# Kernel optimization log

Hardware: AMD Instinct MI355X
Metric: run time of the kernel (lower is better)

The kernel has to match this reference:

```python
import jax, jax.numpy as jnp
import numpy as np

D_MODEL = 1024
NUM_HEADS = 16
DEPTH = D_MODEL // NUM_HEADS
B, S = 2, 2048
NEG = -1e9


def setup_inputs() -> dict:
    key = jax.random.key(0)
    ks = jax.random.split(key, 12)
    sc = 1.0 / np.sqrt(D_MODEL)
    inp = {
        "query": jax.random.normal(ks[0], (B, S, D_MODEL), jnp.float32),
        "key_in": jax.random.normal(ks[1], (B, S, D_MODEL), jnp.float32),
        "value": jax.random.normal(ks[2], (B, S, D_MODEL), jnp.float32),
        # causal mask: 1.0 where attention is disallowed (upper triangle)
        "mask": (1.0 - jnp.tril(jnp.ones((S, S), jnp.float32)))[None, None, :, :],
        "wq": jax.random.normal(ks[3], (D_MODEL, D_MODEL), jnp.float32) * sc,
        "bq": jnp.zeros((D_MODEL,), jnp.float32),
        "wk": jax.random.normal(ks[4], (D_MODEL, D_MODEL), jnp.float32) * sc,
        "bk": jnp.zeros((D_MODEL,), jnp.float32),
        "wv": jax.random.normal(ks[5], (D_MODEL, D_MODEL), jnp.float32) * sc,
        "bv": jnp.zeros((D_MODEL,), jnp.float32),
        "wo": jax.random.normal(ks[6], (D_MODEL, D_MODEL), jnp.float32) * sc,
        "bo": jnp.zeros((D_MODEL,), jnp.float32),
    }
    return inp


def _split_heads(x):
    # [B,S,D] -> [B,H,S,depth]
    b, s, _ = x.shape
    return x.reshape(b, s, NUM_HEADS, DEPTH).transpose(0, 2, 1, 3)


def reference(query, key_in, value, mask, wq, bq, wk, bk, wv, bv, wo, bo):
    q = _split_heads(query @ wq + bq)
    k = _split_heads(key_in @ wk + bk)
    v = _split_heads(value @ wv + bv)
    scale = 1.0 / jnp.sqrt(jnp.asarray(DEPTH, jnp.float32))
    logits = jnp.einsum("bhqd,bhkd->bhqk", q, k) * scale + mask * NEG
    attn = jax.nn.softmax(logits, axis=-1)
    out = jnp.einsum("bhqk,bhkd->bhqd", attn, v)  # [B,H,S,depth]
    out = out.transpose(0, 2, 1, 3).reshape(query.shape[0], -1, D_MODEL)
    return out @ wo + bo
```

## Files before the change

### kernel.cpp

```cpp
#include <hip/hip_runtime.h>
#include <hip/hip_bf16.h>
#include <cstdint>
#include <cstddef>

#define D_MODEL 1024
#define NHEADS  16
#define DEPTH   64
#define BATCH   2
#define SEQ     2048
#define M_TOT   (BATCH*SEQ)
#define QK_SCALE 0.18033688011112042f

typedef __attribute__((ext_vector_type(8)))  __bf16 bf16x8;
typedef __attribute__((ext_vector_type(4)))  float  f32x4;
typedef __attribute__((ext_vector_type(16))) float  f32x16;

__device__ inline unsigned short f2bf(float f){
  unsigned u = __float_as_uint(f);
  u += 0x7FFFu + ((u>>16)&1u);
  return (unsigned short)(u>>16);
}
__device__ inline unsigned cvtpk(float lo, float hi){
  unsigned r;
  asm("v_cvt_pk_bf16_f32 %0, %1, %2" : "=v"(r) : "v"(lo), "v"(hi));
  return r;
}
__device__ inline float fexp2(float x){
  float r;
  asm("v_exp_f32 %0, %1" : "=v"(r) : "v"(x));
  return r;
}
__device__ inline int bswap23(int x){
  return (x & ~12) | ((x & 4) << 1) | ((x & 8) >> 1);
}

#define AS1(p) ((__attribute__((address_space(1))) void*)(p))
#define AS3(p) ((__attribute__((address_space(3))) void*)(p))

__device__ inline void bar_vm4(){
  asm volatile("s_waitcnt vmcnt(4)" ::: "memory");
  __builtin_amdgcn_s_barrier();
  __builtin_amdgcn_sched_barrier(0);
}
__device__ inline void bar_lg(){
  asm volatile("s_waitcnt lgkmcnt(0)" ::: "memory");
  __builtin_amdgcn_s_barrier();
  __builtin_amdgcn_sched_barrier(0);
}

__global__ void tcvt4(const float* __restrict__ w0, const float* __restrict__ w1,
                      const float* __restrict__ w2, const float* __restrict__ w3,
                      unsigned short* o0, unsigned short* o1,
                      unsigned short* o2, unsigned short* o3){
  const float* W = blockIdx.z==0 ? w0 : blockIdx.z==1 ? w1 : blockIdx.z==2 ? w2 : w3;
  unsigned short* Wt = blockIdx.z==0 ? o0 : blockIdx.z==1 ? o1 : blockIdx.z==2 ? o2 : o3;
  const bool perm = (blockIdx.z == 3);
  __shared__ float t[32][33];
  int bx = blockIdx.x*32, by = blockIdx.y*32;
  for (int j = threadIdx.y; j < 32; j += 8)
    t[j][threadIdx.x] = W[(size_t)(by+j)*D_MODEL + bx + threadIdx.x];
  __syncthreads();
  for (int j = threadIdx.y; j < 32; j += 8){
    int col = by + threadIdx.x;
    if (perm) col = bswap23(col);
    Wt[(size_t)(bx+j)*D_MODEL + col] = f2bf(t[threadIdx.x][j]);
  }
}

#define BM 128
#define BN 128
#define BK 32
#define GK 1024

__global__ __launch_bounds__(256,2) void gemm_qkv(
    const float* __restrict__ Xfq, const float* __restrict__ Xfk,
    const float* __restrict__ Xfv,
    const unsigned short* __restrict__ Wq, const unsigned short* __restrict__ Wk,
    const unsigned short* __restrict__ Wv,
    const float* __restrict__ bq, const float* __restrict__ bk, const float* __restrict__ bv,
    unsigned short* Qh, unsigned short* Kh, unsigned short* Vth)
{
  __shared__ __align__(16) short As[BM*BK];
  __shared__ __align__(16) short Bs[2][BN*BK];
  const int z = blockIdx.z;
  const float* Af          = z==0 ? Xfq : z==1 ? Xfk : Xfv;
  const unsigned short* Bt = z==0 ? Wq  : z==1 ? Wk  : Wv;
  const float* bias        = z==0 ? bq  : z==1 ? bk  : bv;

  const int tid = threadIdx.x, lane = tid & 63, wave = tid >> 6;
  const int m0 = blockIdx.x*BM, n0 = blockIdx.y*BN;
  const int wm = wave >> 1, wn = wave & 1;

  f32x4 acc[4][4];
  #pragma unroll
  for (int i=0;i<4;i++)
    #pragma unroll
    for (int j=0;j<4;j++)
      acc[i][j] = (f32x4){0.f,0.f,0.f,0.f};

  const char* Afb   = (const char*)Af + (size_t)m0*GK*4;
  const char* Bbase = (const char*)Bt + (size_t)n0*GK*2;
  const int arow = tid >> 2;
  const int acb  = (tid & 3) * 32;

  float4 alo0[2], ahi0[2], alo1[2], ahi1[2];

#define LOADA(LO, HI, k0) \
  _Pragma("unroll") \
  for (int c=0;c<2;c++){ \
    const char* p_ = Afb + (size_t)(c*64 + arow)*(GK*4) + (size_t)(k0)*4 + acb; \
    LO[c] = *(const float4*)p_; HI[c] = *(const float4*)(p_ + 16); }

#define ISSUEB(t) \
  _Pragma("unroll") \
  for (int c=0;c<2;c++) \
    __builtin_amdgcn_global_load_lds( \
      AS1(Bbase + (size_t)(c*64 + arow)*(GK*2) + (t)*64 + (tid&3)*16), \
      AS3((char*)&Bs[(t)&1][0] + c*4096 + tid*16), 16, 0, 0);

#define CVT_WR(LO, HI) { \
    uint4 pk_[2]; \
    _Pragma("unroll") \
    for (int c=0;c<2;c++){ \
      pk_[c].x = cvtpk(LO[c].x, LO[c].y); pk_[c].y = cvtpk(LO[c].z, LO[c].w); \
      pk_[c].z = cvtpk(HI[c].x, HI[c].y); pk_[c].w = cvtpk(HI[c].z, HI[c].w); } \
    bar_vm4(); \
    _Pragma("unroll") \
    for (int c=0;c<2;c++) *(uint4*)((char*)As + c*4096 + tid*16) = pk_[c]; \
    bar_lg(); }

#define CVT_WR_SYNC(LO, HI) { \
    uint4 pk_[2]; \
    _Pragma("unroll") \
    for (int c=0;c<2;c++){ \
      pk_[c].x = cvtpk(LO[c].x, LO[c].y); pk_[c].y = cvtpk(LO[c].z, LO[c].w); \
      pk_[c].z = cvtpk(HI[c].x, HI[c].y); pk_[c].w = cvtpk(HI[c].z, HI[c].w); } \
    __syncthreads(); \
    _Pragma("unroll") \
    for (int c=0;c<2;c++) *(uint4*)((char*)As + c*4096 + tid*16) = pk_[c]; \
    __syncthreads(); }

#define MFMA_PHASE(BUF) { \
    bf16x8 af_[4], bfv_[4]; \
    _Pragma("unroll") \
    for (int i=0;i<4;i++) \
      af_[i] = *(const bf16x8*)((const char*)As + (wm*64+i*16+(lane&15))*64 + (lane>>4)*16); \
    _Pragma("unroll") \
    for (int j=0;j<4;j++) \
      bfv_[j] = *(const bf16x8*)((const char*)&Bs[BUF][0] + (wn*64+j*16+(lane&15))*64 + (lane>>4)*16); \
    _Pragma("unroll") \
    for (int i=0;i<4;i++) \
      _Pragma("unroll") \
      for (int j=0;j<4;j++) \
        acc[i][j] = __builtin_amdgcn_mfma_f32_16x16x32_bf16(af_[i], bfv_[j], acc[i][j], 0,0,0); }

  ISSUEB(0)
  __builtin_amdgcn_sched_barrier(0);
  LOADA(alo0, ahi0, 0)
  LOADA(alo1, ahi1, 32)

  #pragma unroll 1
  for (int k0 = 0; k0 < 960; k0 += 64){
    const int t = k0 >> 5;
    CVT_WR(alo0, ahi0)
    ISSUEB(t+1)
    __builtin_amdgcn_sched_barrier(0);
    LOADA(alo0, ahi0, k0+64)
    MFMA_PHASE(t&1)
    CVT_WR(alo1, ahi1)
    ISSUEB(t+2)
    __builtin_amdgcn_sched_barrier(0);
    LOADA(alo1, ahi1, k0+96)
    MFMA_PHASE((t+1)&1)
  }
  CVT_WR_SYNC(alo0, ahi0)
  ISSUEB(31)
  MFMA_PHASE(0)
  CVT_WR_SYNC(alo1, ahi1)
  MFMA_PHASE(1)

  #pragma unroll
  for (int i=0;i<4;i++)
    #pragma unroll
    for (int j=0;j<4;j++)
      #pragma unroll
      for (int r=0;r<4;r++){
        int gr = m0 + wm*64 + i*16 + (lane>>4)*4 + r;
        int gc = n0 + wn*64 + j*16 + (lane&15);
        float v = acc[i][j][r] + bias[gc];
        int b = gr>>11, s = gr&2047, h = gc>>6, d = gc&63;
        if (z == 0){
          v *= QK_SCALE;
          Qh[(((size_t)(b*NHEADS+h))*SEQ + s)*DEPTH + d] = f2bf(v);
        } else if (z == 1){
          Kh[(((size_t)(b*NHEADS+h))*SEQ + s)*DEPTH + d] = f2bf(v);
        } else {
          int sp = bswap23(s);
          Vth[(((size_t)(b*NHEADS+h))*DEPTH + d)*SEQ + sp] = f2bf(v);
        }
      }
#undef LOADA
#undef ISSUEB
#undef CVT_WR
#undef CVT_WR_SYNC
#undef MFMA_PHASE
}

#define BM2 64
__global__ __launch_bounds__(256,2) void gemm_out(
    const unsigned short* __restrict__ A,
    const unsigned short* __restrict__ Bt,
    const float* __restrict__ bias,
    float* __restrict__ Cout)
{
  __shared__ __align__(16) short As[2][BM2*BK];
  __shared__ __align__(16) short Bs[2][BN*BK];
  const int tid = threadIdx.x, lane = tid & 63, wave = tid >> 6;
  const int m0 = blockIdx.x*BM2, n0 = blockIdx.y*BN;
  const int wm = wave >> 1, wn = wave & 1;

  f32x4 acc[2][4];
  #pragma unroll
  for (int i=0;i<2;i++)
    #pragma unroll
    for (int j=0;j<4;j++)
      acc[i][j] = (f32x4){0.f,0.f,0.f,0.f};

  const char* Abase = (const char*)A + (size_t)m0*GK*2;
  const char* Bbase = (const char*)Bt + (size_t)n0*GK*2;

  auto STAGE = [&](int t){
    __builtin_amdgcn_global_load_lds(
      AS1(Abase + (size_t)(tid>>2)*(GK*2) + t*64 + (tid&3)*16),
      AS3((char*)&As[t&1][0] + tid*16), 16, 0, 0);
    #pragma unroll
    for (int c=0;c<2;c++)
      __builtin_amdgcn_global_load_lds(
        AS1(Bbase + (size_t)(c*64 + (tid>>2))*(GK*2) + t*64 + (tid&3)*16),
        AS3((char*)&Bs[t&1][0] + c*4096 + tid*16), 16, 0, 0);
  };

  STAGE(0);
  #pragma unroll 1
  for (int t = 0; t < 32; ++t){
    __syncthreads();
    if (t+1 < 32) STAGE(t+1);
    bf16x8 af[2], bfv[4];
    #pragma unroll
    for (int i=0;i<2;i++)
      af[i] = *(const bf16x8*)((const char*)&As[t&1][0] + (wm*32 + i*16 + (lane&15))*64 + (lane>>4)*16);
    #pragma unroll
    for (int j=0;j<4;j++)
      bfv[j] = *(const bf16x8*)((const char*)&Bs[t&1][0] + (wn*64 + j*16 + (lane&15))*64 + (lane>>4)*16);
    #pragma unroll
    for (int i=0;i<2;i++)
      #pragma unroll
      for (int j=0;j<4;j++)
        acc[i][j] = __builtin_amdgcn_mfma_f32_16x16x32_bf16(af[i], bfv[j], acc[i][j], 0,0,0);
  }

  #pragma unroll
  for (int i=0;i<2;i++)
    #pragma unroll
    for (int j=0;j<4;j++)
      #pragma unroll
      for (int r=0;r<4;r++){
        int gr = m0 + wm*32 + i*16 + (lane>>4)*4 + r;
        int gc = n0 + wn*64 + j*16 + (lane&15);
        Cout[(size_t)gr*D_MODEL + gc] = acc[i][j][r] + bias[gc];
      }
}

__global__ __launch_bounds__(512,4) void attn_fwd(
  const unsigned short* __restrict__ Qh,
  const unsigned short* __restrict__ Kh,
  const unsigned short* __restrict__ Vt,
  unsigned short* __restrict__ AO)
{
  __shared__ __align__(16) short Ks[2][4096];
  __shared__ __align__(16) short Vs[2][4096];
  __shared__ float cbS[2][128];

  const int tid = threadIdx.x, lane = tid & 63, w = tid >> 6;
  const int h = lane >> 5, ql = lane & 31;
  const int qh = w & 1, kh = (w >> 1) & 1, tl = w >> 2;
  const int pj = blockIdx.x, bh = blockIdx.y;
  const size_t hb = (size_t)bh * SEQ * DEPTH;
  const char* Kb = (const char*)(Kh + hb);
  const char* Vb = (const char*)(Vt + hb);
  const unsigned short* Qb = Qh + hb;
  const int bb = bh >> 4, hd = bh & 15;
  const int swz = (ql & 7) << 4;

  auto STAGE = [&](int buf, int t){
    const int kv0 = t*64;
    #pragma unroll
    for (int i=0;i<2;i++){
      int c = (w&3)*2 + i;
      int x = c*1024 + lane*16;
      int row = x >> 7;
      int cb = (x & 127) ^ ((row&7)<<4);
      if (w < 4)
        __builtin_amdgcn_global_load_lds(
          AS1(Kb + (size_t)(kv0+row)*128 + cb),
          AS3((char*)&Ks[buf][0] + c*1024), 16, 0, 0);
      else
        __builtin_amdgcn_global_load_lds(
          AS1(Vb + ((size_t)row*SEQ + kv0)*2 + cb),
          AS3((char*)&Vs[buf][0] + c*1024), 16, 0, 0);
    }
  };

  const int jtw = tl ? pj : (31 - pj);
  const int Q0 = jtw*64 + qh*32;
  const int qmax = Q0 + 31;
  const int Tblock = 32 - pj;

  bf16x8 qreg[4];
  {
    const unsigned short* qp = Qb + (size_t)(Q0 + ql)*DEPTH + h*8;
    #pragma unroll
    for (int c=0;c<4;c++) qreg[c] = *(const bf16x8*)(qp + c*16);
  }

  f32x16 oacc[2];
  #pragma unroll
  for (int dh=0;dh<2;dh++)
    #pragma unroll
    for (int r=0;r<16;r++) oacc[dh][r] = 0.f;
  float s = 0.f;

  STAGE(0, 0);
  __syncthreads();
  int cur = 0;

  #pragma unroll 1
  for (int t = 0; t < Tblock; ++t){
    if (t+1 < Tblock) STAGE(cur^1, t+1);
    const int kvb = t*64 + kh*32;

    if (kvb <= qmax){
      f32x16 sa;
      #pragma unroll
      for (int r=0;r<16;r++) sa[r] = -16.0f;
      #pragma unroll
      for (int c=0;c<4;c++){
        bf16x8 kf = *(const bf16x8*)((const char*)&Ks[cur][0]
                      + (kh*32 + ql)*128 + ((32*c + 16*h) ^ swz));
        sa = __builtin_amdgcn_mfma_f32_32x32x16_bf16(kf, qreg[c], sa, 0,0,0);
      }

      if (kvb + 31 > Q0){
        const int qg = Q0 + ql - kvb;
        #pragma unroll
        for (int r=0;r<16;r++){
          int pos = (r&3) + 8*(r>>2) + 4*h;
          sa[r] = (pos > qg) ? -1e9f : sa[r];
        }
      }

      float s0=0.f, s1=0.f, s2=0.f, s3=0.f;
      #pragma unroll
      for (int r=0;r<16;r++){
        float p = fexp2(sa[r]);
        sa[r] = p;
        if ((r&3)==0) s0 += p; else if ((r&3)==1) s1 += p;
        else if ((r&3)==2) s2 += p; else s3 += p;
      }
      s += (s0+s1)+(s2+s3);

      bf16x8 pw[2];
      #pragma unroll
      for (int ks=0;ks<2;ks++){
        const int mm = 8*ks;
        union { unsigned u[4]; bf16x8 v; } pk;
        pk.u[0] = cvtpk(sa[mm+0], sa[mm+1]);
        pk.u[1] = cvtpk(sa[mm+2], sa[mm+3]);
        pk.u[2] = cvtpk(sa[mm+4], sa[mm+5]);
        pk.u[3] = cvtpk(sa[mm+6], sa[mm+7]);
        pw[ks] = pk.v;
      }

      #pragma unroll
      for (int ks=0;ks<2;ks++){
        #pragma unroll
        for (int dh=0;dh<2;dh++){
          bf16x8 vf = *(const bf16x8*)((const char*)&Vs[cur][0]
                        + (dh*32 + ql)*128 + ((kh*64 + ks*32 + 16*h) ^ swz));
          oacc[dh] = __builtin_amdgcn_mfma_f32_32x32x16_bf16(vf, pw[ks], oacc[dh], 0,0,0);
        }
      }
    }

    __syncthreads();
    cur ^= 1;
  }

  float* cbO  = (tl == 0) ? (float*)&Ks[0][0] : (float*)&Vs[0][0];
  float* cbSp = &cbS[tl][0];
  if (kh == 1){
    #pragma unroll
    for (int dh=0;dh<2;dh++)
      #pragma unroll
      for (int r=0;r<16;r++)
        cbO[(dh*16+r)*128 + qh*64 + lane] = oacc[dh][r];
    cbSp[qh*64 + lane] = s;
  }
  __syncthreads();
  if (kh == 0){
    #pragma unroll
    for (int dh=0;dh<2;dh++)
      #pragma unroll
      for (int r=0;r<16;r++)
        oacc[dh][r] += cbO[(dh*16+r)*128 + qh*64 + lane];
    s += cbSp[qh*64 + lane];
    float st = s + __shfl_xor(s, 32, 64);
    float inv = 1.0f / st;
    #pragma unroll
    for (int dh=0;dh<2;dh++)
      #pragma unroll
      for (int r=0;r<16;r++) oacc[dh][r] *= inv;

    unsigned short* orow = AO + ((size_t)bb*SEQ + (Q0 + ql))*D_MODEL + hd*DEPTH;
    #pragma unroll
    for (int dh=0;dh<2;dh++)
      #pragma unroll
      for (int g=0; g<2; g++){
        uint4 st4;
        st4.x = cvtpk(oacc[dh][8*g+0], oacc[dh][8*g+1]);
        st4.y = cvtpk(oacc[dh][8*g+2], oacc[dh][8*g+3]);
        st4.z = cvtpk(oacc[dh][8*g+4], oacc[dh][8*g+5]);
        st4.w = cvtpk(oacc[dh][8*g+6], oacc[dh][8*g+7]);
        *(uint4*)(orow + dh*32 + g*16 + h*8) = st4;
      }
  }
}

extern "C" void kernel_launch(void* const* d_in, const int* in_sizes, int n_in,
                              void* d_out, int out_size, void* d_ws, size_t ws_size,
                              hipStream_t stream) {
  const float* query  = (const float*)d_in[0];
  const float* key_in = (const float*)d_in[1];
  const float* value  = (const float*)d_in[2];
  const float* wq = (const float*)d_in[4];
  const float* bq = (const float*)d_in[5];
  const float* wk = (const float*)d_in[6];
  const float* bk = (const float*)d_in[7];
  const float* wv = (const float*)d_in[8];
  const float* bv = (const float*)d_in[9];
  const float* wo = (const float*)d_in[10];
  const float* bo = (const float*)d_in[11];

  char* ws = (char*)d_ws;
  const size_t MB = 1u<<20;
  unsigned short* Wtq = (unsigned short*)(ws + 24*MB);
  unsigned short* Wtk = (unsigned short*)(ws + 26*MB);
  unsigned short* Wtv = (unsigned short*)(ws + 28*MB);
  unsigned short* Wto = (unsigned short*)(ws + 30*MB);
  unsigned short* Qh  = (unsigned short*)(ws + 32*MB);
  unsigned short* Kh  = (unsigned short*)(ws + 40*MB);
  unsigned short* Vth = (unsigned short*)(ws + 48*MB);
  unsigned short* AO  = (unsigned short*)(ws + 56*MB);

  tcvt4<<<dim3(32,32,4), dim3(32,8), 0, stream>>>(wq, wk, wv, wo, Wtq, Wtk, Wtv, Wto);

  gemm_qkv<<<dim3(M_TOT/BM, D_MODEL/BN, 3), 256, 0, stream>>>(
      query, key_in, value, Wtq, Wtk, Wtv, bq, bk, bv, Qh, Kh, Vth);

  attn_fwd<<<dim3(16, BATCH*NHEADS), 512, 0, stream>>>(Qh, Kh, Vth, AO);

  gemm_out<<<dim3(M_TOT/BM2, D_MODEL/BN), 256, 0, stream>>>(AO, Wto, bo, (float*)d_out);
}
```

Baseline: 107.6 us.

## Load QKV GEMM weight fragments directly into registers, dropping LDS B buffers

The QKV projection GEMM no longer stages weight tiles through double-buffered shared memory with async global-to-LDS loads. Each wave now loads its B fragments straight from global memory into registers, double-buffered in registers, and the loop is restructured with a guarded tail instead of an epilogue. Freeing the LDS allows launch bounds to target 3 blocks per CU. The cost is redundant global reads of B across the two wm waves, more VGPR pressure, and a loss of the async LDS copy overlap.

```diff
diff --git a/kernel.cpp b/kernel.cpp
--- a/kernel.cpp
+++ b/kernel.cpp
@@ -37,11 +37,6 @@
 #define AS1(p) ((__attribute__((address_space(1))) void*)(p))
 #define AS3(p) ((__attribute__((address_space(3))) void*)(p))
 
-__device__ inline void bar_vm4(){
-  asm volatile("s_waitcnt vmcnt(4)" ::: "memory");
-  __builtin_amdgcn_s_barrier();
-  __builtin_amdgcn_sched_barrier(0);
-}
 __device__ inline void bar_lg(){
   asm volatile("s_waitcnt lgkmcnt(0)" ::: "memory");
   __builtin_amdgcn_s_barrier();
@@ -72,7 +67,7 @@
 #define BK 32
 #define GK 1024
 
-__global__ __launch_bounds__(256,2) void gemm_qkv(
+__global__ __launch_bounds__(256,3) void gemm_qkv(
     const float* __restrict__ Xfq, const float* __restrict__ Xfk,
     const float* __restrict__ Xfv,
     const unsigned short* __restrict__ Wq, const unsigned short* __restrict__ Wk,
@@ -81,7 +76,6 @@
     unsigned short* Qh, unsigned short* Kh, unsigned short* Vth)
 {
   __shared__ __align__(16) short As[BM*BK];
-  __shared__ __align__(16) short Bs[2][BN*BK];
   const int z = blockIdx.z;
   const float* Af          = z==0 ? Xfq : z==1 ? Xfk : Xfv;
   const unsigned short* Bt = z==0 ? Wq  : z==1 ? Wk  : Wv;
@@ -104,6 +98,7 @@
   const int acb  = (tid & 3) * 32;
 
   float4 alo0[2], ahi0[2], alo1[2], ahi1[2];
+  uint4 b0[4], b1[4];
 
 #define LOADA(LO, HI, k0) \
   _Pragma("unroll") \
@@ -111,12 +106,12 @@
     const char* p_ = Afb + (size_t)(c*64 + arow)*(GK*4) + (size_t)(k0)*4 + acb; \
     LO[c] = *(const float4*)p_; HI[c] = *(const float4*)(p_ + 16); }
 
-#define ISSUEB(t) \
+#define LOADB(B, k) \
   _Pragma("unroll") \
-  for (int c=0;c<2;c++) \
-    __builtin_amdgcn_global_load_lds( \
-      AS1(Bbase + (size_t)(c*64 + arow)*(GK*2) + (t)*64 + (tid&3)*16), \
-      AS3((char*)&Bs[(t)&1][0] + c*4096 + tid*16), 16, 0, 0);
+  for (int j=0;j<4;j++){ \
+    const char* pb_ = Bbase + (size_t)(wn*64 + j*16 + (lane&15))*(GK*2) \
+                      + (size_t)(k)*2 + (lane>>4)*16; \
+    B[j] = *(const uint4*)pb_; }
 
 #define CVT_WR(LO, HI) { \
     uint4 pk_[2]; \
@@ -124,60 +119,39 @@
     for (int c=0;c<2;c++){ \
       pk_[c].x = cvtpk(LO[c].x, LO[c].y); pk_[c].y = cvtpk(LO[c].z, LO[c].w); \
       pk_[c].z = cvtpk(HI[c].x, HI[c].y); pk_[c].w = cvtpk(HI[c].z, HI[c].w); } \
-    bar_vm4(); \
+    bar_lg();                           \
     _Pragma("unroll") \
     for (int c=0;c<2;c++) *(uint4*)((char*)As + c*4096 + tid*16) = pk_[c]; \
-    bar_lg(); }
-
-#define CVT_WR_SYNC(LO, HI) { \
-    uint4 pk_[2]; \
-    _Pragma("unroll") \
-    for (int c=0;c<2;c++){ \
-      pk_[c].x = cvtpk(LO[c].x, LO[c].y); pk_[c].y = cvtpk(LO[c].z, LO[c].w); \
-      pk_[c].z = cvtpk(HI[c].x, HI[c].y); pk_[c].w = cvtpk(HI[c].z, HI[c].w); } \
-    __syncthreads(); \
-    _Pragma("unroll") \
-    for (int c=0;c<2;c++) *(uint4*)((char*)As + c*4096 + tid*16) = pk_[c]; \
-    __syncthreads(); }
-
-#define MFMA_PHASE(BUF) { \
-    bf16x8 af_[4], bfv_[4]; \
+    bar_lg();                           }
+
+#define MFMA_PHASE(B) { \
+    bf16x8 af_[4]; \
     _Pragma("unroll") \
     for (int i=0;i<4;i++) \
       af_[i] = *(const bf16x8*)((const char*)As + (wm*64+i*16+(lane&15))*64 + (lane>>4)*16); \
     _Pragma("unroll") \
-    for (int j=0;j<4;j++) \
-      bfv_[j] = *(const bf16x8*)((const char*)&Bs[BUF][0] + (wn*64+j*16+(lane&15))*64 + (lane>>4)*16); \
-    _Pragma("unroll") \
-    for (int i=0;i<4;i++) \
+    for (int i=0;i<4;i++){ \
       _Pragma("unroll") \
-      for (int j=0;j<4;j++) \
-        acc[i][j] = __builtin_amdgcn_mfma_f32_16x16x32_bf16(af_[i], bfv_[j], acc[i][j], 0,0,0); }
-
-  ISSUEB(0)
-  __builtin_amdgcn_sched_barrier(0);
+      for (int j=0;j<4;j++){ \
+        bf16x8 bv_ = *(const bf16x8*)&B[j]; \
+        acc[i][j] = __builtin_amdgcn_mfma_f32_16x16x32_bf16(af_[i], bv_, acc[i][j], 0,0,0); } } }
+
   LOADA(alo0, ahi0, 0)
+  LOADB(b0, 0)
   LOADA(alo1, ahi1, 32)
+  LOADB(b1, 32)
 
   #pragma unroll 1
-  for (int k0 = 0; k0 < 960; k0 += 64){
-    const int t = k0 >> 5;
+  for (int k0 = 0; k0 < GK; k0 += 64){
     CVT_WR(alo0, ahi0)
-    ISSUEB(t+1)
-    __builtin_amdgcn_sched_barrier(0);
-    LOADA(alo0, ahi0, k0+64)
-    MFMA_PHASE(t&1)
+    if (k0 + 64 < GK) LOADA(alo0, ahi0, k0+64)
+    MFMA_PHASE(b0)
+    if (k0 + 64 < GK) LOADB(b0, k0+64)
     CVT_WR(alo1, ahi1)
-    ISSUEB(t+2)
-    __builtin_amdgcn_sched_barrier(0);
-    LOADA(alo1, ahi1, k0+96)
-    MFMA_PHASE((t+1)&1)
-  }
-  CVT_WR_SYNC(alo0, ahi0)
-  ISSUEB(31)
-  MFMA_PHASE(0)
-  CVT_WR_SYNC(alo1, ahi1)
-  MFMA_PHASE(1)
+    if (k0 + 96 < GK) LOADA(alo1, ahi1, k0+96)
+    MFMA_PHASE(b1)
+    if (k0 + 96 < GK) LOADB(b1, k0+96)
+  }
 
   #pragma unroll
   for (int i=0;i<4;i++)
@@ -200,9 +174,8 @@
         }
       }
 #undef LOADA
-#undef ISSUEB
+#undef LOADB
 #undef CVT_WR
-#undef CVT_WR_SYNC
 #undef MFMA_PHASE
 }
 
```

New measurement: 129.9 us. +20.7%, slower.
